# Optimization experiments

Hardware: AMD Instinct MI355X
Metric: run time of the kernel (lower is better)

Reference implementation:

```python
import jax, jax.numpy as jnp
import numpy as np

DIM, E_DIM, HID = 512, 1024, 256
N_EXP, N_MIC, TOP_K, TOP_K_MIC = 8, 325, 2, 8
EPS_LN = 1e-5


def _layernorm(x, g, b):
    mu = x.mean(-1, keepdims=True)
    var = ((x - mu) ** 2).mean(-1, keepdims=True)
    return (x - mu) / jnp.sqrt(var + EPS_LN) * g + b


def setup_inputs() -> dict:
    key = jax.random.key(0)
    ks = jax.random.split(key, 20)
    s = 0.02
    return {
        "x": jax.random.normal(ks[0], (2, 512, DIM), jnp.float32),
        "router_w": jax.random.normal(ks[1], (N_EXP, DIM), jnp.float32) * s,
        "router_b": jnp.zeros((N_EXP,), jnp.float32),
        "exp_w1": jax.random.normal(ks[2], (N_EXP, E_DIM, DIM), jnp.float32) * s,
        "exp_b1": jnp.zeros((N_EXP, E_DIM), jnp.float32),
        "exp_w2": jax.random.normal(ks[3], (N_EXP, DIM, E_DIM), jnp.float32) * s,
        "exp_b2": jnp.zeros((N_EXP, DIM), jnp.float32),
        "mrouter_w": jax.random.normal(ks[4], (N_MIC, DIM), jnp.float32) * s,
        "mrouter_b": jnp.zeros((N_MIC,), jnp.float32),
        "mic_w1": jax.random.normal(ks[5], (N_MIC, HID, DIM), jnp.float32) * s,
        "mic_b1": jnp.zeros((N_MIC, HID), jnp.float32),
        "mic_w2": jax.random.normal(ks[6], (N_MIC, DIM, HID), jnp.float32) * s,
        "mic_b2": jnp.zeros((N_MIC, DIM), jnp.float32),
        "mic_g": jnp.ones((N_MIC, DIM), jnp.float32),
        "mic_beta": jnp.zeros((N_MIC, DIM), jnp.float32),
        "norm_g": jnp.ones((DIM,), jnp.float32),
        "norm_b": jnp.zeros((DIM,), jnp.float32),
    }


def _forward(x, router_w, router_b, exp_w1, exp_b1, exp_w2, exp_b2,
             mrouter_w, mrouter_b, mic_w1, mic_b1, mic_w2, mic_b2,
             mic_g, mic_beta, norm_g, norm_b):
    B, S, D = x.shape
    xf = x.reshape(-1, D)  # [T, D]

    # ---- expert routing (top-2 of 8) ----
    probs = jax.nn.softmax(xf @ router_w.T + router_b, axis=-1)
    topp, topi = jax.lax.top_k(probs, TOP_K)
    topp = topp / (topp.sum(-1, keepdims=True) + 1e-8)

    # dense compute over 8 experts, combine with top-k weights
    h = jax.nn.gelu(jnp.einsum('td,ehd->teh', xf, exp_w1) + exp_b1, approximate=False)
    ye = jnp.einsum('teh,edh->ted', h, exp_w2) + exp_b2  # [T, E, D]
    comb_w = (jax.nn.one_hot(topi, N_EXP, dtype=xf.dtype) * topp[..., None]).sum(1)  # [T, E]
    eo = jnp.einsum('te,ted->td', comb_w, ye)

    # ---- micro routing (top-8 of 325) ----
    mprobs = jax.nn.softmax(eo @ mrouter_w.T + mrouter_b, axis=-1)
    mtopp, mtopi = jax.lax.top_k(mprobs, TOP_K_MIC)
    mtopp = mtopp / (mtopp.sum(-1, keepdims=True) + 1e-8)

    def micro_slot(eo, p, idx):
        # gather per-token micro params, batched GEMV dispatch
        hm = jax.nn.gelu(jnp.einsum('td,thd->th', eo, mic_w1[idx]) + mic_b1[idx],
                         approximate=False)
        ym = jnp.einsum('th,tdh->td', hm, mic_w2[idx]) + mic_b2[idx]
        n = _layernorm(eo + ym, mic_g[idx], mic_beta[idx])
        return p[:, None] * n

    micro_slot = jax.checkpoint(micro_slot, static_argnums=())
    mo = jnp.zeros_like(eo)
    for k in range(TOP_K_MIC):  # small fixed loop over slots
        mo = mo + micro_slot(eo, mtopp[:, k], mtopi[:, k])

    combined = (eo + 0.1 * mo).reshape(B, S, D)
    return _layernorm(combined, norm_g, norm_b)


def reference(x, router_w, router_b, exp_w1, exp_b1, exp_w2, exp_b2,
              mrouter_w, mrouter_b, mic_w1, mic_b1, mic_w2, mic_b2,
              mic_g, mic_beta, norm_g, norm_b):
    return _forward(x, router_w, router_b, exp_w1, exp_b1, exp_w2, exp_b2,
                    mrouter_w, mrouter_b, mic_w1, mic_b1, mic_w2, mic_b2,
                    mic_g, mic_beta, norm_g, norm_b)
```

## Files before the change

### kernel.cpp

```cpp
#include <hip/hip_runtime.h>
#include <hip/hip_bf16.h>
#include <math.h>

#define T_TOK 1024
#define DIMM  512
#define EDIM  1024
#define HIDD  256
#define NEXP  8
#define NMIC  325
#define E8TILES 264
#define MTILES  840

typedef __attribute__((ext_vector_type(8))) short bf16x8;
typedef __attribute__((ext_vector_type(4))) float f32x4;

__device__ __forceinline__ float dot4(float4 a, float4 b) {
    return a.x*b.x + a.y*b.y + a.z*b.z + a.w*b.w;
}
__device__ __forceinline__ float gelu_exact(float x) {
    return 0.5f * x * (1.0f + erff(x * 0.70710678118654752f));
}
__device__ __forceinline__ float wave_sum(float v) {
    #pragma unroll
    for (int o = 32; o; o >>= 1) v += __shfl_xor(v, o);
    return v;
}
__device__ __forceinline__ short f2bf(float f) {
    union { __hip_bfloat16 h; short s; } u;
    u.h = __float2bfloat16(f);
    return u.s;
}
__device__ __forceinline__ bf16x8 cvt8(float4 a, float4 b) {
    bf16x8 r;
    r[0]=f2bf(a.x); r[1]=f2bf(a.y); r[2]=f2bf(a.z); r[3]=f2bf(a.w);
    r[4]=f2bf(b.x); r[5]=f2bf(b.y); r[6]=f2bf(b.z); r[7]=f2bf(b.w);
    return r;
}

__global__ void k_router(const float* __restrict__ x, const float* __restrict__ rw,
                         const float* __restrict__ rb, int* __restrict__ eidx,
                         float* __restrict__ ew, int* __restrict__ ecnt) {
    int wave = threadIdx.x >> 6, lane = threadIdx.x & 63;
    int t = blockIdx.x * 4 + wave;
    if (t >= T_TOK) return;
    const float* xr = x + (size_t)t * DIMM;
    float xv[8];
    #pragma unroll
    for (int j = 0; j < 8; ++j) xv[j] = xr[lane + 64*j];
    float p[NEXP];
    #pragma unroll
    for (int e = 0; e < NEXP; ++e) {
        const float* wr = rw + (size_t)e * DIMM;
        float a = 0.f;
        #pragma unroll
        for (int j = 0; j < 8; ++j) a += xv[j] * wr[lane + 64*j];
        p[e] = wave_sum(a) + rb[e];
    }
    float m = p[0];
    #pragma unroll
    for (int e = 1; e < NEXP; ++e) m = fmaxf(m, p[e]);
    float Z = 0.f;
    #pragma unroll
    for (int e = 0; e < NEXP; ++e) { p[e] = expf(p[e] - m); Z += p[e]; }
    #pragma unroll
    for (int e = 0; e < NEXP; ++e) p[e] /= Z;
    int i1 = 0; float v1 = p[0];
    #pragma unroll
    for (int e = 1; e < NEXP; ++e) if (p[e] > v1) { v1 = p[e]; i1 = e; }
    int i2 = -1; float v2 = -1.f;
    #pragma unroll
    for (int e = 0; e < NEXP; ++e) if (e != i1 && p[e] > v2) { v2 = p[e]; i2 = e; }
    float s = v1 + v2 + 1e-8f;
    if (lane == 0) {
        eidx[t*2] = i1; eidx[t*2+1] = i2;
        ew[t*2] = v1 / s; ew[t*2+1] = v2 / s;
        atomicAdd(&ecnt[i1], 1); atomicAdd(&ecnt[i2], 1);
    }
}

__global__ void k_scan(const int* __restrict__ cnt, int n, int pm,
                       int* __restrict__ off, int* __restrict__ cur,
                       int2* __restrict__ tiles, int* __restrict__ ntile) {
    __shared__ int s[512], s2[512];
    int tid = threadIdx.x;
    int v  = (tid < n) ? cnt[tid] : 0;
    int tc = (v + pm - 1) / pm;
    s[tid] = v; s2[tid] = tc;
    __syncthreads();
    for (int d = 1; d < 512; d <<= 1) {
        int a = (tid >= d) ? s[tid-d] : 0;
        int b = (tid >= d) ? s2[tid-d] : 0;
        __syncthreads();
        s[tid] += a; s2[tid] += b;
        __syncthreads();
    }
    int myoff = s[tid] - v, tb = s2[tid] - tc;
    if (tid < n) { off[tid] = myoff; cur[tid] = myoff; }
    if (tid == n-1) off[n] = s[tid];
    if (tid == 511) *ntile = s2[511];
    for (int j = 0; j < tc; ++j) tiles[tb + j] = make_int2(tid, myoff + j*pm);
}

__global__ void k_scatter(const int* __restrict__ idx, const float* __restrict__ w,
                          int total, int S, int* __restrict__ cur,
                          int* __restrict__ ptok, float* __restrict__ pw) {
    int g = blockIdx.x * blockDim.x + threadIdx.x;
    if (g >= total) return;
    int t = g / S;
    int e = idx[g];
    int pos = atomicAdd(&cur[e], 1);
    ptok[pos] = t; pw[pos] = w[g];
}

__global__ __launch_bounds__(256) void k_effn1(
    const float* __restrict__ x, const float* __restrict__ w1, const float* __restrict__ b1,
    const int2* __restrict__ tiles, const int* __restrict__ ntile,
    const int* __restrict__ eoff, const int* __restrict__ ep_tok,
    float* __restrict__ hbuf) {
    if ((int)blockIdx.x >= *ntile) return;
    int2 tl = tiles[blockIdx.x];
    int e = tl.x, pbase = tl.y;
    int m = min(8, eoff[e+1] - pbase);
    __shared__ float4 xs[8][128];
    __shared__ int tok_s[8];
    int tid = threadIdx.x;
    if (tid < 8) tok_s[tid] = ep_tok[pbase + ((tid < m) ? tid : 0)];
    __syncthreads();
    const float4* x4 = (const float4*)x;
    for (int q = tid; q < 8*128; q += 256) {
        int i = q >> 7, k = q & 127;
        xs[i][k] = x4[(size_t)tok_s[i] * 128 + k];
    }
    __syncthreads();
    int c = blockIdx.y * 256 + tid;
    const float4* wr = (const float4*)(w1 + ((size_t)e * EDIM + c) * DIMM);
    float acc[8];
    #pragma unroll
    for (int i = 0; i < 8; ++i) acc[i] = 0.f;
    for (int kk = 0; kk < 128; ++kk) {
        float4 wv = wr[kk];
        #pragma unroll
        for (int i = 0; i < 8; ++i) acc[i] += dot4(wv, xs[i][kk]);
    }
    float bb = b1[(size_t)e * EDIM + c];
    for (int i = 0; i < m; ++i)
        hbuf[(size_t)(pbase + i) * EDIM + c] = gelu_exact(acc[i] + bb);
}

__global__ __launch_bounds__(256) void k_effn2(
    const float* __restrict__ hbuf, const float* __restrict__ w2, const float* __restrict__ b2,
    const int2* __restrict__ tiles, const int* __restrict__ ntile,
    const int* __restrict__ eoff, const int* __restrict__ ep_tok, const float* __restrict__ ep_w,
    float* __restrict__ eo) {
    if ((int)blockIdx.x >= *ntile) return;
    int2 tl = tiles[blockIdx.x];
    int e = tl.x, pbase = tl.y;
    int m = min(8, eoff[e+1] - pbase);
    int kc = blockIdx.z;
    __shared__ float4 hs[8][128];
    __shared__ int tok_s[8];
    __shared__ float pw_s[8];
    int tid = threadIdx.x;
    if (tid < 8) {
        int ok = tid < m;
        tok_s[tid] = ok ? ep_tok[pbase + tid] : 0;
        pw_s[tid]  = ok ? ep_w[pbase + tid] : 0.f;
    }
    __syncthreads();
    const float4* h4 = (const float4*)hbuf;
    for (int q = tid; q < 8*128; q += 256) {
        int i = q >> 7, k = q & 127;
        hs[i][k] = h4[(size_t)(pbase + ((i < m) ? i : 0)) * 256 + kc * 128 + k];
    }
    __syncthreads();
    int c = blockIdx.y * 256 + tid;
    const float4* wr = (const float4*)(w2 + ((size_t)e * DIMM + c) * EDIM + (size_t)kc * 512);
    float acc[8];
    #pragma unroll
    for (int i = 0; i < 8; ++i) acc[i] = 0.f;
    for (int kk = 0; kk < 128; ++kk) {
        float4 wv = wr[kk];
        #pragma unroll
        for (int i = 0; i < 8; ++i) acc[i] += dot4(wv, hs[i][kk]);
    }
    float bb = (kc == 0) ? b2[(size_t)e * DIMM + c] : 0.f;
    for (int i = 0; i < m; ++i) {
        float val = (acc[i] + bb) * pw_s[i];
        atomicAdd(&eo[(size_t)tok_s[i] * DIMM + c], val);
    }
}

__global__ __launch_bounds__(384) void k_mlog(
    const float* __restrict__ eo, const float* __restrict__ mw, const float* __restrict__ mb,
    float* __restrict__ mlog) {
    int t0 = blockIdx.x * 4;
    __shared__ float4 es[4][128];
    int tid = threadIdx.x;
    const float4* eo4 = (const float4*)eo;
    for (int q = tid; q < 4*128; q += 384) {
        int i = q >> 7, k = q & 127;
        es[i][k] = eo4[(size_t)(t0 + i) * 128 + k];
    }
    __syncthreads();
    if (tid < NMIC) {
        const float4* wr = (const float4*)(mw + (size_t)tid * DIMM);
        float acc[4] = {0.f, 0.f, 0.f, 0.f};
        for (int kk = 0; kk < 128; ++kk) {
            float4 wv = wr[kk];
            #pragma unroll
            for (int i = 0; i < 4; ++i) acc[i] += dot4(wv, es[i][kk]);
        }
        float bb = mb[tid];
        #pragma unroll
        for (int i = 0; i < 4; ++i) mlog[(size_t)(t0 + i) * NMIC + tid] = acc[i] + bb;
    }
}

__global__ void k_mtop(const float* __restrict__ mlog, int* __restrict__ mtopi,
                       float* __restrict__ mtopp, int* __restrict__ mcnt) {
    int wave = threadIdx.x >> 6, lane = threadIdx.x & 63;
    int t = blockIdx.x * 4 + wave;
    if (t >= T_TOK) return;
    float v[6]; int vi[6];
    #pragma unroll
    for (int j = 0; j < 6; ++j) {
        int n = lane + 64*j;
        vi[j] = n;
        v[j] = (n < NMIC) ? mlog[(size_t)t * NMIC + n] : -1e30f;
    }
    float M = v[0];
    #pragma unroll
    for (int j = 1; j < 6; ++j) M = fmaxf(M, v[j]);
    #pragma unroll
    for (int o = 32; o; o >>= 1) M = fmaxf(M, __shfl_xor(M, o));
    float Z = 0.f;
    #pragma unroll
    for (int j = 0; j < 6; ++j) Z += expf(v[j] - M);
    Z = wave_sum(Z);
    float bk[8]; int bi[8];
    for (int k = 0; k < 8; ++k) {
        float lv = v[0]; int li = vi[0];
        #pragma unroll
        for (int j = 1; j < 6; ++j)
            if (v[j] > lv) { lv = v[j]; li = vi[j]; }
        #pragma unroll
        for (int o = 32; o; o >>= 1) {
            float ov = __shfl_xor(lv, o); int oi = __shfl_xor(li, o);
            if (ov > lv || (ov == lv && oi < li)) { lv = ov; li = oi; }
        }
        bk[k] = expf(lv - M) / Z; bi[k] = li;
        #pragma unroll
        for (int j = 0; j < 6; ++j) if (vi[j] == li) v[j] = -1e30f;
    }
    float s = 0.f;
    #pragma unroll
    for (int k = 0; k < 8; ++k) s += bk[k];
    s += 1e-8f;
    if (lane == 0) {
        for (int k = 0; k < 8; ++k) {
            mtopi[t*8 + k] = bi[k];
            mtopp[t*8 + k] = bk[k] / s;
            atomicAdd(&mcnt[bi[k]], 1);
        }
    }
}

__global__ __launch_bounds__(256, 4) void k_micro(
    const float* __restrict__ eo, const float* __restrict__ w1, const float* __restrict__ b1,
    const float* __restrict__ w2, const float* __restrict__ b2,
    const float* __restrict__ g, const float* __restrict__ beta,
    const int2* __restrict__ tiles, const int* __restrict__ ntile,
    const int* __restrict__ moff, const int* __restrict__ mp_tok, const float* __restrict__ mp_w,
    float* __restrict__ mo) {
    if ((int)blockIdx.x >= *ntile) return;
    int2 tl = tiles[blockIdx.x];
    int mi = tl.x, pbase = tl.y;
    int pm = min(16, moff[mi+1] - pbase);
    __shared__ __align__(16) char smem[34816];
    short* hf  = (short*)smem;
    short* eof = (short*)(smem + 8192);
    float* R   = (float*)smem;
    __shared__ int tok_s[16];
    __shared__ float pw_s[16];
    int tid = threadIdx.x;
    if (tid < 16) {
        int ok = tid < pm;
        tok_s[tid] = mp_tok[pbase + (ok ? tid : 0)];
        pw_s[tid]  = ok ? mp_w[pbase + tid] : 0.f;
    }
    __syncthreads();
    int m0 = tid & 15;
    const float4* eorow = (const float4*)(eo + (size_t)tok_s[m0] * DIMM);
    for (int kk = tid >> 4; kk < 128; kk += 16) {
        float4 v = eorow[kk];
        int off = ((kk >> 3) * 512) + ((((kk >> 1) & 3) * 16 + m0) * 8) + ((kk & 1) * 4);
        short4 s4; s4.x = f2bf(v.x); s4.y = f2bf(v.y); s4.z = f2bf(v.z); s4.w = f2bf(v.w);
        *(short4*)(eof + off) = s4;
    }
    __syncthreads();
    int wave = tid >> 6, lane = tid & 63;
    int quad = lane >> 4, lcol = lane & 15;
    f32x4 zero = {0.f, 0.f, 0.f, 0.f};
    f32x4 accA[4];
    #pragma unroll
    for (int q = 0; q < 4; ++q) accA[q] = zero;
    const float* w1base = w1 + (size_t)mi * HIDD * DIMM;
    for (int ks = 0; ks < 16; ++ks) {
        bf16x8 a = *(bf16x8*)(eof + ks*512 + lane*8);
        int kb = ks*32 + quad*8;
        #pragma unroll
        for (int q = 0; q < 4; ++q) {
            int n = wave*64 + q*16 + lcol;
            const float* wp = w1base + (size_t)n * DIMM + kb;
            float4 wa = *(const float4*)wp;
            float4 wb = *(const float4*)(wp + 4);
            accA[q] = __builtin_amdgcn_mfma_f32_16x16x32_bf16(a, cvt8(wa, wb), accA[q], 0, 0, 0);
        }
    }
    #pragma unroll
    for (int q = 0; q < 4; ++q) {
        int h = wave*64 + q*16 + lcol;
        float bb = b1[(size_t)mi * HIDD + h];
        int obase = ((h >> 5) * 512) + (((h >> 3) & 3) * 16) * 8 + (h & 7);
        #pragma unroll
        for (int r = 0; r < 4; ++r) {
            int mm = quad*4 + r;
            hf[obase + mm*8] = f2bf(gelu_exact(accA[q][r] + bb));
        }
    }
    __syncthreads();
    f32x4 accB[8];
    #pragma unroll
    for (int q = 0; q < 8; ++q) accB[q] = zero;
    const float* w2base = w2 + (size_t)mi * DIMM * HIDD;
    for (int ks = 0; ks < 8; ++ks) {
        bf16x8 a = *(bf16x8*)(hf + ks*512 + lane*8);
        int kb = ks*32 + quad*8;
        #pragma unroll
        for (int q = 0; q < 8; ++q) {
            int d = wave*128 + q*16 + lcol;
            const float* wp = w2base + (size_t)d * HIDD + kb;
            float4 wa = *(const float4*)wp;
            float4 wb = *(const float4*)(wp + 4);
            accB[q] = __builtin_amdgcn_mfma_f32_16x16x32_bf16(a, cvt8(wa, wb), accB[q], 0, 0, 0);
        }
    }
    __syncthreads();
    #pragma unroll
    for (int q = 0; q < 8; ++q) {
        int d = wave*128 + q*16 + lcol;
        float bb = b2[(size_t)mi * DIMM + d];
        #pragma unroll
        for (int r = 0; r < 4; ++r) {
            int mm = quad*4 + r;
            R[mm*520 + d] = accB[q][r] + bb;
        }
    }
    __syncthreads();
    for (int i = wave; i < pm; i += 4) {
        int t = tok_s[i];
        const float* eort = eo + (size_t)t * DIMM;
        float vv[8];
        float sum = 0.f;
        #pragma unroll
        for (int j = 0; j < 8; ++j) {
            int d = lane + 64*j;
            vv[j] = R[i*520 + d] + eort[d];
            sum += vv[j];
        }
        sum = wave_sum(sum);
        float mu = sum * (1.f/512.f);
        float var = 0.f;
        #pragma unroll
        for (int j = 0; j < 8; ++j) { float d0 = vv[j] - mu; var += d0*d0; }
        var = wave_sum(var) * (1.f/512.f);
        float rstd = rsqrtf(var + 1e-5f);
        float p = pw_s[i];
        #pragma unroll
        for (int j = 0; j < 8; ++j) {
            int d = lane + 64*j;
            float nj = (vv[j] - mu) * rstd * g[(size_t)mi * DIMM + d] + beta[(size_t)mi * DIMM + d];
            atomicAdd(&mo[(size_t)t * DIMM + d], p * nj);
        }
    }
}

__global__ void k_final(const float* __restrict__ eo, const float* __restrict__ mo,
                        const float* __restrict__ g, const float* __restrict__ b,
                        float* __restrict__ out) {
    int wave = threadIdx.x >> 6, lane = threadIdx.x & 63;
    int t = blockIdx.x * 4 + wave;
    if (t >= T_TOK) return;
    float vv[8];
    float sum = 0.f;
    #pragma unroll
    for (int j = 0; j < 8; ++j) {
        int d = lane + 64*j;
        vv[j] = eo[(size_t)t * DIMM + d] + 0.1f * mo[(size_t)t * DIMM + d];
        sum += vv[j];
    }
    sum = wave_sum(sum);
    float mu = sum * (1.f/512.f);
    float var = 0.f;
    #pragma unroll
    for (int j = 0; j < 8; ++j) { float d0 = vv[j] - mu; var += d0*d0; }
    var = wave_sum(var) * (1.f/512.f);
    float rstd = rsqrtf(var + 1e-5f);
    #pragma unroll
    for (int j = 0; j < 8; ++j) {
        int d = lane + 64*j;
        out[(size_t)t * DIMM + d] = (vv[j] - mu) * rstd * g[d] + b[d];
    }
}

extern "C" void kernel_launch(void* const* d_in, const int* in_sizes, int n_in,
                              void* d_out, int out_size, void* d_ws, size_t ws_size,
                              hipStream_t stream) {
    const float* x    = (const float*)d_in[0];
    const float* rw   = (const float*)d_in[1];
    const float* rb   = (const float*)d_in[2];
    const float* ew1  = (const float*)d_in[3];
    const float* eb1  = (const float*)d_in[4];
    const float* ew2  = (const float*)d_in[5];
    const float* eb2  = (const float*)d_in[6];
    const float* mrw  = (const float*)d_in[7];
    const float* mrb  = (const float*)d_in[8];
    const float* mw1  = (const float*)d_in[9];
    const float* mb1  = (const float*)d_in[10];
    const float* mw2  = (const float*)d_in[11];
    const float* mb2  = (const float*)d_in[12];
    const float* mg   = (const float*)d_in[13];
    const float* mbeta= (const float*)d_in[14];
    const float* ng   = (const float*)d_in[15];
    const float* nb   = (const float*)d_in[16];
    float* out = (float*)d_out;

    char* w = (char*)d_ws;
    auto alloc = [&](size_t bytes) -> char* {
        char* p = w;
        w += (bytes + 255) & ~(size_t)255;
        return p;
    };
    float* eo    = (float*)alloc((size_t)T_TOK * DIMM * 4);
    float* mo    = (float*)alloc((size_t)T_TOK * DIMM * 4);
    float* hbuf  = (float*)alloc((size_t)2048 * EDIM * 4);
    float* mlog  = (float*)alloc((size_t)T_TOK * NMIC * 4);
    float* ewts  = (float*)alloc(2048 * 4);
    float* mtopp = (float*)alloc(8192 * 4);
    float* ep_w  = (float*)alloc(2048 * 4);
    float* mp_w  = (float*)alloc(8192 * 4);
    int*   eidx  = (int*)alloc(2048 * 4);
    int*   mtopi = (int*)alloc(8192 * 4);
    int*   cnts  = (int*)alloc((NEXP + NMIC) * 4);
    int*   ecnt  = cnts;
    int*   mcnt  = cnts + NEXP;
    int*   eoff  = (int*)alloc((NEXP + 1) * 4);
    int*   ecur  = (int*)alloc(NEXP * 4);
    int*   moff  = (int*)alloc((NMIC + 1) * 4);
    int*   mcur  = (int*)alloc(NMIC * 4);
    int2*  etile = (int2*)alloc(E8TILES * 8);
    int2*  mtile = (int2*)alloc(MTILES * 8);
    int*   entile= (int*)alloc(4);
    int*   mntile= (int*)alloc(4);
    int*   ep_tok= (int*)alloc(2048 * 4);
    int*   mp_tok= (int*)alloc(8192 * 4);

    hipMemsetAsync(eo, 0, (size_t)2 * T_TOK * DIMM * 4, stream);
    hipMemsetAsync(cnts, 0, (NEXP + NMIC) * 4, stream);

    k_router <<<T_TOK/4, 256, 0, stream>>>(x, rw, rb, eidx, ewts, ecnt);
    k_scan   <<<1, 512, 0, stream>>>(ecnt, NEXP, 8, eoff, ecur, etile, entile);
    k_scatter<<<(T_TOK*2 + 255)/256, 256, 0, stream>>>(eidx, ewts, T_TOK*2, 2, ecur, ep_tok, ep_w);
    k_effn1  <<<dim3(E8TILES, 4, 1), 256, 0, stream>>>(x, ew1, eb1, etile, entile, eoff, ep_tok, hbuf);
    k_effn2  <<<dim3(E8TILES, 2, 2), 256, 0, stream>>>(hbuf, ew2, eb2, etile, entile, eoff, ep_tok, ep_w, eo);
    k_mlog   <<<T_TOK/4, 384, 0, stream>>>(eo, mrw, mrb, mlog);
    k_mtop   <<<T_TOK/4, 256, 0, stream>>>(mlog, mtopi, mtopp, mcnt);
    k_scan   <<<1, 512, 0, stream>>>(mcnt, NMIC, 16, moff, mcur, mtile, mntile);
    k_scatter<<<(T_TOK*8 + 255)/256, 256, 0, stream>>>(mtopi, mtopp, T_TOK*8, 8, mcur, mp_tok, mp_w);
    k_micro  <<<MTILES, 256, 0, stream>>>(eo, mw1, mb1, mw2, mb2, mg, mbeta,
                                          mtile, mntile, moff, mp_tok, mp_w, mo);
    k_final  <<<T_TOK/4, 256, 0, stream>>>(eo, mo, ng, nb, out);
}
```

Measured before the change: 719.4 us.

## Fuse scan with scatter, widen blocks to 512 threads, prefetch micro-expert weights

Merges the prefix-scan and scatter kernels into one single-block kernel, which removes two launches. The expert FFN, micro-router and micro-expert kernels move to 512- or 768-thread blocks with fewer blocks or less work per wave. The micro-expert kernel now register double-buffers its weight loads ahead of the MFMAs to hide global latency. The single-block scatter serialises atomics that previously ran across many blocks, and the larger blocks change occupancy and register pressure.

```diff
diff --git a/kernel.cpp b/kernel.cpp
--- a/kernel.cpp
+++ b/kernel.cpp
@@ -78,9 +78,12 @@
     }
 }
 
-__global__ void k_scan(const int* __restrict__ cnt, int n, int pm,
-                       int* __restrict__ off, int* __restrict__ cur,
-                       int2* __restrict__ tiles, int* __restrict__ ntile) {
+__global__ __launch_bounds__(512) void k_scan_scatter(
+    const int* __restrict__ cnt, int n, int pm,
+    const int* __restrict__ idx, const float* __restrict__ wts, int total, int S,
+    int* __restrict__ off, int* __restrict__ cur,
+    int2* __restrict__ tiles, int* __restrict__ ntile,
+    int* __restrict__ ptok, float* __restrict__ pw) {
     __shared__ int s[512], s2[512];
     int tid = threadIdx.x;
     int v  = (tid < n) ? cnt[tid] : 0;
@@ -99,20 +102,16 @@
     if (tid == n-1) off[n] = s[tid];
     if (tid == 511) *ntile = s2[511];
     for (int j = 0; j < tc; ++j) tiles[tb + j] = make_int2(tid, myoff + j*pm);
-}
-
-__global__ void k_scatter(const int* __restrict__ idx, const float* __restrict__ w,
-                          int total, int S, int* __restrict__ cur,
-                          int* __restrict__ ptok, float* __restrict__ pw) {
-    int g = blockIdx.x * blockDim.x + threadIdx.x;
-    if (g >= total) return;
-    int t = g / S;
-    int e = idx[g];
-    int pos = atomicAdd(&cur[e], 1);
-    ptok[pos] = t; pw[pos] = w[g];
-}
-
-__global__ __launch_bounds__(256) void k_effn1(
+    __syncthreads();
+    for (int g = tid; g < total; g += 512) {
+        int t = g / S;
+        int e = idx[g];
+        int pos = atomicAdd(&cur[e], 1);
+        ptok[pos] = t; pw[pos] = wts[g];
+    }
+}
+
+__global__ __launch_bounds__(512) void k_effn1(
     const float* __restrict__ x, const float* __restrict__ w1, const float* __restrict__ b1,
     const int2* __restrict__ tiles, const int* __restrict__ ntile,
     const int* __restrict__ eoff, const int* __restrict__ ep_tok,
@@ -127,16 +126,17 @@
     if (tid < 8) tok_s[tid] = ep_tok[pbase + ((tid < m) ? tid : 0)];
     __syncthreads();
     const float4* x4 = (const float4*)x;
-    for (int q = tid; q < 8*128; q += 256) {
+    for (int q = tid; q < 8*128; q += 512) {
         int i = q >> 7, k = q & 127;
         xs[i][k] = x4[(size_t)tok_s[i] * 128 + k];
     }
     __syncthreads();
-    int c = blockIdx.y * 256 + tid;
+    int c = blockIdx.y * 512 + tid;
     const float4* wr = (const float4*)(w1 + ((size_t)e * EDIM + c) * DIMM);
     float acc[8];
     #pragma unroll
     for (int i = 0; i < 8; ++i) acc[i] = 0.f;
+    #pragma unroll 4
     for (int kk = 0; kk < 128; ++kk) {
         float4 wv = wr[kk];
         #pragma unroll
@@ -147,7 +147,7 @@
         hbuf[(size_t)(pbase + i) * EDIM + c] = gelu_exact(acc[i] + bb);
 }
 
-__global__ __launch_bounds__(256) void k_effn2(
+__global__ __launch_bounds__(512) void k_effn2(
     const float* __restrict__ hbuf, const float* __restrict__ w2, const float* __restrict__ b2,
     const int2* __restrict__ tiles, const int* __restrict__ ntile,
     const int* __restrict__ eoff, const int* __restrict__ ep_tok, const float* __restrict__ ep_w,
@@ -156,7 +156,7 @@
     int2 tl = tiles[blockIdx.x];
     int e = tl.x, pbase = tl.y;
     int m = min(8, eoff[e+1] - pbase);
-    int kc = blockIdx.z;
+    int kc = blockIdx.y;
     __shared__ float4 hs[8][128];
     __shared__ int tok_s[8];
     __shared__ float pw_s[8];
@@ -168,16 +168,17 @@
     }
     __syncthreads();
     const float4* h4 = (const float4*)hbuf;
-    for (int q = tid; q < 8*128; q += 256) {
+    for (int q = tid; q < 8*128; q += 512) {
         int i = q >> 7, k = q & 127;
         hs[i][k] = h4[(size_t)(pbase + ((i < m) ? i : 0)) * 256 + kc * 128 + k];
     }
     __syncthreads();
-    int c = blockIdx.y * 256 + tid;
+    int c = tid;
     const float4* wr = (const float4*)(w2 + ((size_t)e * DIMM + c) * EDIM + (size_t)kc * 512);
     float acc[8];
     #pragma unroll
     for (int i = 0; i < 8; ++i) acc[i] = 0.f;
+    #pragma unroll 4
     for (int kk = 0; kk < 128; ++kk) {
         float4 wv = wr[kk];
         #pragma unroll
@@ -190,29 +191,26 @@
     }
 }
 
-__global__ __launch_bounds__(384) void k_mlog(
+__global__ __launch_bounds__(768) void k_mlog(
     const float* __restrict__ eo, const float* __restrict__ mw, const float* __restrict__ mb,
     float* __restrict__ mlog) {
-    int t0 = blockIdx.x * 4;
-    __shared__ float4 es[4][128];
+    int t0 = blockIdx.x * 2;
+    __shared__ float4 es[2][128];
     int tid = threadIdx.x;
     const float4* eo4 = (const float4*)eo;
-    for (int q = tid; q < 4*128; q += 384) {
-        int i = q >> 7, k = q & 127;
+    if (tid < 256) {
+        int i = tid >> 7, k = tid & 127;
         es[i][k] = eo4[(size_t)(t0 + i) * 128 + k];
     }
     __syncthreads();
-    if (tid < NMIC) {
-        const float4* wr = (const float4*)(mw + (size_t)tid * DIMM);
-        float acc[4] = {0.f, 0.f, 0.f, 0.f};
-        for (int kk = 0; kk < 128; ++kk) {
-            float4 wv = wr[kk];
-            #pragma unroll
-            for (int i = 0; i < 4; ++i) acc[i] += dot4(wv, es[i][kk]);
-        }
-        float bb = mb[tid];
-        #pragma unroll
-        for (int i = 0; i < 4; ++i) mlog[(size_t)(t0 + i) * NMIC + tid] = acc[i] + bb;
+    int half = (tid >= 384) ? 1 : 0;
+    int n = tid - half * 384;
+    if (n < NMIC) {
+        const float4* wr = (const float4*)(mw + (size_t)n * DIMM);
+        float acc = 0.f;
+        #pragma unroll 4
+        for (int kk = 0; kk < 128; ++kk) acc += dot4(wr[kk], es[half][kk]);
+        mlog[(size_t)(t0 + half) * NMIC + n] = acc + mb[n];
     }
 }
 
@@ -265,7 +263,7 @@
     }
 }
 
-__global__ __launch_bounds__(256, 4) void k_micro(
+__global__ __launch_bounds__(512, 4) void k_micro(
     const float* __restrict__ eo, const float* __restrict__ w1, const float* __restrict__ b1,
     const float* __restrict__ w2, const float* __restrict__ b2,
     const float* __restrict__ g, const float* __restrict__ beta,
@@ -291,7 +289,7 @@
     __syncthreads();
     int m0 = tid & 15;
     const float4* eorow = (const float4*)(eo + (size_t)tok_s[m0] * DIMM);
-    for (int kk = tid >> 4; kk < 128; kk += 16) {
+    for (int kk = tid >> 4; kk < 128; kk += 32) {
         float4 v = eorow[kk];
         int off = ((kk >> 3) * 512) + ((((kk >> 1) & 3) * 16 + m0) * 8) + ((kk & 1) * 4);
         short4 s4; s4.x = f2bf(v.x); s4.y = f2bf(v.y); s4.z = f2bf(v.z); s4.w = f2bf(v.w);
@@ -301,25 +299,34 @@
     int wave = tid >> 6, lane = tid & 63;
     int quad = lane >> 4, lcol = lane & 15;
     f32x4 zero = {0.f, 0.f, 0.f, 0.f};
-    f32x4 accA[4];
-    #pragma unroll
-    for (int q = 0; q < 4; ++q) accA[q] = zero;
-    const float* w1base = w1 + (size_t)mi * HIDD * DIMM;
+    f32x4 accA[2];
+    accA[0] = zero; accA[1] = zero;
+    const float* w1q = w1 + (size_t)mi * HIDD * DIMM + quad * 8;
+    const float* wA0 = w1q + (size_t)(wave*32      + lcol) * DIMM;
+    const float* wA1 = w1q + (size_t)(wave*32 + 16 + lcol) * DIMM;
+    float4 cA[4];
+    cA[0] = *(const float4*)(wA0); cA[1] = *(const float4*)(wA0 + 4);
+    cA[2] = *(const float4*)(wA1); cA[3] = *(const float4*)(wA1 + 4);
+    #pragma unroll
     for (int ks = 0; ks < 16; ++ks) {
+        float4 nA[4];
+        if (ks < 15) {
+            const float* p0 = wA0 + (ks+1)*32;
+            const float* p1 = wA1 + (ks+1)*32;
+            nA[0] = *(const float4*)p0; nA[1] = *(const float4*)(p0 + 4);
+            nA[2] = *(const float4*)p1; nA[3] = *(const float4*)(p1 + 4);
+        }
         bf16x8 a = *(bf16x8*)(eof + ks*512 + lane*8);
-        int kb = ks*32 + quad*8;
-        #pragma unroll
-        for (int q = 0; q < 4; ++q) {
-            int n = wave*64 + q*16 + lcol;
-            const float* wp = w1base + (size_t)n * DIMM + kb;
-            float4 wa = *(const float4*)wp;
-            float4 wb = *(const float4*)(wp + 4);
-            accA[q] = __builtin_amdgcn_mfma_f32_16x16x32_bf16(a, cvt8(wa, wb), accA[q], 0, 0, 0);
-        }
-    }
-    #pragma unroll
-    for (int q = 0; q < 4; ++q) {
-        int h = wave*64 + q*16 + lcol;
+        accA[0] = __builtin_amdgcn_mfma_f32_16x16x32_bf16(a, cvt8(cA[0], cA[1]), accA[0], 0, 0, 0);
+        accA[1] = __builtin_amdgcn_mfma_f32_16x16x32_bf16(a, cvt8(cA[2], cA[3]), accA[1], 0, 0, 0);
+        if (ks < 15) {
+            #pragma unroll
+            for (int j = 0; j < 4; ++j) cA[j] = nA[j];
+        }
+    }
+    #pragma unroll
+    for (int q = 0; q < 2; ++q) {
+        int h = wave*32 + q*16 + lcol;
         float bb = b1[(size_t)mi * HIDD + h];
         int obase = ((h >> 5) * 512) + (((h >> 3) & 3) * 16) * 8 + (h & 7);
         #pragma unroll
@@ -329,26 +336,43 @@
         }
     }
     __syncthreads();
-    f32x4 accB[8];
-    #pragma unroll
-    for (int q = 0; q < 8; ++q) accB[q] = zero;
-    const float* w2base = w2 + (size_t)mi * DIMM * HIDD;
+    f32x4 accB[4];
+    #pragma unroll
+    for (int q = 0; q < 4; ++q) accB[q] = zero;
+    const float* w2q = w2 + (size_t)mi * DIMM * HIDD + quad * 8;
+    const float* wB[4];
+    #pragma unroll
+    for (int q = 0; q < 4; ++q) wB[q] = w2q + (size_t)(wave*64 + q*16 + lcol) * HIDD;
+    float4 cB[8];
+    #pragma unroll
+    for (int q = 0; q < 4; ++q) {
+        cB[2*q]   = *(const float4*)(wB[q]);
+        cB[2*q+1] = *(const float4*)(wB[q] + 4);
+    }
+    #pragma unroll
     for (int ks = 0; ks < 8; ++ks) {
+        float4 nB[8];
+        if (ks < 7) {
+            #pragma unroll
+            for (int q = 0; q < 4; ++q) {
+                const float* p = wB[q] + (ks+1)*32;
+                nB[2*q]   = *(const float4*)p;
+                nB[2*q+1] = *(const float4*)(p + 4);
+            }
+        }
         bf16x8 a = *(bf16x8*)(hf + ks*512 + lane*8);
-        int kb = ks*32 + quad*8;
-        #pragma unroll
-        for (int q = 0; q < 8; ++q) {
-            int d = wave*128 + q*16 + lcol;
-            const float* wp = w2base + (size_t)d * HIDD + kb;
-            float4 wa = *(const float4*)wp;
-            float4 wb = *(const float4*)(wp + 4);
-            accB[q] = __builtin_amdgcn_mfma_f32_16x16x32_bf16(a, cvt8(wa, wb), accB[q], 0, 0, 0);
-        }
-    }
-    __syncthreads();
-    #pragma unroll
-    for (int q = 0; q < 8; ++q) {
-        int d = wave*128 + q*16 + lcol;
+        #pragma unroll
+        for (int q = 0; q < 4; ++q)
+            accB[q] = __builtin_amdgcn_mfma_f32_16x16x32_bf16(a, cvt8(cB[2*q], cB[2*q+1]), accB[q], 0, 0, 0);
+        if (ks < 7) {
+            #pragma unroll
+            for (int j = 0; j < 8; ++j) cB[j] = nB[j];
+        }
+    }
+    __syncthreads();
+    #pragma unroll
+    for (int q = 0; q < 4; ++q) {
+        int d = wave*64 + q*16 + lcol;
         float bb = b2[(size_t)mi * DIMM + d];
         #pragma unroll
         for (int r = 0; r < 4; ++r) {
@@ -357,7 +381,7 @@
         }
     }
     __syncthreads();
-    for (int i = wave; i < pm; i += 4) {
+    for (int i = wave; i < pm; i += 8) {
         int t = tok_s[i];
         const float* eort = eo + (size_t)t * DIMM;
         float vv[8];
@@ -469,15 +493,15 @@
     hipMemsetAsync(cnts, 0, (NEXP + NMIC) * 4, stream);
 
     k_router <<<T_TOK/4, 256, 0, stream>>>(x, rw, rb, eidx, ewts, ecnt);
-    k_scan   <<<1, 512, 0, stream>>>(ecnt, NEXP, 8, eoff, ecur, etile, entile);
-    k_scatter<<<(T_TOK*2 + 255)/256, 256, 0, stream>>>(eidx, ewts, T_TOK*2, 2, ecur, ep_tok, ep_w);
-    k_effn1  <<<dim3(E8TILES, 4, 1), 256, 0, stream>>>(x, ew1, eb1, etile, entile, eoff, ep_tok, hbuf);
-    k_effn2  <<<dim3(E8TILES, 2, 2), 256, 0, stream>>>(hbuf, ew2, eb2, etile, entile, eoff, ep_tok, ep_w, eo);
-    k_mlog   <<<T_TOK/4, 384, 0, stream>>>(eo, mrw, mrb, mlog);
+    k_scan_scatter<<<1, 512, 0, stream>>>(ecnt, NEXP, 8, eidx, ewts, T_TOK*2, 2,
+                                          eoff, ecur, etile, entile, ep_tok, ep_w);
+    k_effn1  <<<dim3(E8TILES, 2), 512, 0, stream>>>(x, ew1, eb1, etile, entile, eoff, ep_tok, hbuf);
+    k_effn2  <<<dim3(E8TILES, 2), 512, 0, stream>>>(hbuf, ew2, eb2, etile, entile, eoff, ep_tok, ep_w, eo);
+    k_mlog   <<<T_TOK/2, 768, 0, stream>>>(eo, mrw, mrb, mlog);
     k_mtop   <<<T_TOK/4, 256, 0, stream>>>(mlog, mtopi, mtopp, mcnt);
-    k_scan   <<<1, 512, 0, stream>>>(mcnt, NMIC, 16, moff, mcur, mtile, mntile);
-    k_scatter<<<(T_TOK*8 + 255)/256, 256, 0, stream>>>(mtopi, mtopp, T_TOK*8, 8, mcur, mp_tok, mp_w);
-    k_micro  <<<MTILES, 256, 0, stream>>>(eo, mw1, mb1, mw2, mb2, mg, mbeta,
+    k_scan_scatter<<<1, 512, 0, stream>>>(mcnt, NMIC, 16, mtopi, mtopp, T_TOK*8, 8,
+                                          moff, mcur, mtile, mntile, mp_tok, mp_w);
+    k_micro  <<<MTILES, 512, 0, stream>>>(eo, mw1, mb1, mw2, mb2, mg, mbeta,
                                           mtile, mntile, moff, mp_tok, mp_w, mo);
     k_final  <<<T_TOK/4, 256, 0, stream>>>(eo, mo, ng, nb, out);
 }
```

After: 826.9 us. 1.15x slower.
